# Optimization experiments

Measured on AMD Instinct MI355X. Metric: run time of the kernel, lower is better.

The kernel has to match this reference:

```python
import jax, jax.numpy as jnp
import numpy as np

N_HEAD = 16

def setup_inputs() -> dict:
    key = jax.random.key(0)
    k1, k2, k3, k4 = jax.random.split(key, 4)
    B, S, D = 2, 2048, 1024
    seq_in = jax.random.normal(k1, (B, S, D), dtype=jnp.float32)
    # nn.Linear weights, shape [out_features, in_features], y = x @ W.T
    scale = 1.0 / np.sqrt(D)
    Wq = jax.random.normal(k2, (D, D), dtype=jnp.float32) * scale
    Wk = jax.random.normal(k3, (D, D), dtype=jnp.float32) * scale
    Wv = jax.random.normal(k4, (D, D), dtype=jnp.float32) * scale
    return {"seq_in": seq_in, "Wq": Wq, "Wk": Wk, "Wv": Wv}

def reference(seq_in, Wq, Wk, Wv):
    B, S, D = seq_in.shape
    H = N_HEAD
    Dh = D // H
    scale = float(D) ** 0.5  # NOTE: sqrt(model_dim), as in the source
    # Linear projections: y = x @ W.T
    q = jnp.einsum('bsd,ed->bse', seq_in, Wq)
    k = jnp.einsum('bsd,ed->bse', seq_in, Wk)
    v = jnp.einsum('bsd,ed->bse', seq_in, Wv)
    # Faithful to source: .view(B, n_head, -1, head_dim) splits the SEQ dim,
    # not a transpose-based head split.
    q = q.reshape(B, H, S, Dh)
    k = k.reshape(B, H, S, Dh)
    v = v.reshape(B, H, S, Dh)
    sim_score = jnp.einsum('bhqd,bhkd->bhqk', q, k) / scale  # [B,H,S,S]
    sim_score = jax.nn.softmax(sim_score, axis=-1)
    # dropout is identity in eval mode
    self_attn = jnp.einsum('bhqk,bhkd->bhqd', sim_score, v)  # [B,H,S,Dh]
    self_attn = jnp.transpose(self_attn, (0, 2, 1, 3)).reshape(B, S, H * Dh)
    return (self_attn, sim_score)
```

## Files before the change

kernel.cpp:

```cpp
#include <hip/hip_runtime.h>
#include <hip/hip_bf16.h>

typedef __attribute__((ext_vector_type(8))) short short8;
typedef __attribute__((ext_vector_type(4))) float f32x4;
typedef __attribute__((ext_vector_type(4))) unsigned short u16x4;
typedef __attribute__((ext_vector_type(8))) unsigned short u16x8;

#define INV_SCALE 0.03125f

__device__ __forceinline__ unsigned short f2bf(float f) {
  unsigned u = __float_as_uint(f);
  u += 0x7fffu + ((u >> 16) & 1u);
  return (unsigned short)(u >> 16);
}

__global__ __launch_bounds__(512) void qkv_proj(
    const float* __restrict__ X, const float* __restrict__ Wq,
    const float* __restrict__ Wk, const float* __restrict__ Wv,
    unsigned short* __restrict__ ws) {
  const int mt = blockIdx.x, nt = blockIdx.y, z = blockIdx.z;
  const float* __restrict__ W = (z == 0) ? Wq : (z == 1) ? Wk : Wv;
  unsigned short* __restrict__ out = ws + (size_t)z * 4096 * 1024;

  __shared__ unsigned short As[128][72];
  __shared__ unsigned short Bs[128][72];

  const int tid = threadIdx.x;
  const int wave = tid >> 6, lane = tid & 63;
  const int lq = lane & 15, lg = lane >> 4;

  f32x4 acc[8] = {};

  for (int kt = 0; kt < 1024; kt += 64) {
    {
      const int row0 = tid >> 4;
      const int col  = (tid & 15) * 4;
#pragma unroll
      for (int i = 0; i < 4; ++i) {
        const int row = row0 + 32 * i;
        float4 a = *(const float4*)(X + (size_t)(mt * 128 + row) * 1024 + kt + col);
        float4 b = *(const float4*)(W + (size_t)(nt * 128 + row) * 1024 + kt + col);
        u16x4 ah = {f2bf(a.x), f2bf(a.y), f2bf(a.z), f2bf(a.w)};
        u16x4 bh = {f2bf(b.x), f2bf(b.y), f2bf(b.z), f2bf(b.w)};
        *(u16x4*)&As[row][col] = ah;
        *(u16x4*)&Bs[row][col] = bh;
      }
    }
    __syncthreads();
#pragma unroll
    for (int ks = 0; ks < 2; ++ks) {
      short8 af = *(const short8*)&As[wave * 16 + lq][ks * 32 + lg * 8];
#pragma unroll
      for (int n = 0; n < 8; ++n) {
        short8 bf = *(const short8*)&Bs[n * 16 + lq][ks * 32 + lg * 8];
        acc[n] = __builtin_amdgcn_mfma_f32_16x16x32_bf16(af, bf, acc[n], 0, 0, 0);
      }
    }
    __syncthreads();
  }
#pragma unroll
  for (int n = 0; n < 8; ++n)
#pragma unroll
    for (int r = 0; r < 4; ++r) {
      const int row = mt * 128 + wave * 16 + lg * 4 + r;
      const int col = nt * 128 + n * 16 + lq;
      out[(size_t)row * 1024 + col] = f2bf(acc[n][r]);
    }
}

__global__ __launch_bounds__(512) void mha_attn(
    const unsigned short* __restrict__ ws, float* __restrict__ out) {
  const int qb = blockIdx.x;
  const int bh = blockIdx.y;
  const int b = bh >> 4, h = bh & 15;

  const unsigned short* __restrict__ Qg = ws + ((size_t)b * 2048 + h * 128) * 1024;
  const unsigned short* __restrict__ Kg = Qg + (size_t)4096 * 1024;
  const unsigned short* __restrict__ Vg = Qg + (size_t)2 * 4096 * 1024;

  float* __restrict__ simout =
      out + (size_t)4194304 + ((size_t)bh * 2048 + (size_t)qb * 128) * 2048;
  float* __restrict__ attnout = out + (size_t)b * 2048 * 1024 + h * 64;

  __shared__ unsigned short Ks[128][72];
  __shared__ unsigned short VTs[64][136];
  __shared__ unsigned short Ps[8][16][136];

  const int tid = threadIdx.x;
  const int wave = tid >> 6, lane = tid & 63;
  const int lq = lane & 15, lg = lane >> 4;

  short8 qf[2];
  {
    const unsigned short* qrow = Qg + (size_t)(qb * 128 + wave * 16 + lq) * 64;
    qf[0] = *(const short8*)(qrow + lg * 8);
    qf[1] = *(const short8*)(qrow + 32 + lg * 8);
  }

  float m[4], l[4];
#pragma unroll
  for (int r = 0; r < 4; ++r) { m[r] = -1e30f; l[r] = 0.f; }

  for (int kt = 0; kt < 16; ++kt) {
#pragma unroll
    for (int i = 0; i < 2; ++i) {
      const int slot = tid + 512 * i;
      const int row = slot >> 3, cg = (slot & 7) * 8;
      u16x8 v = *(const u16x8*)(Kg + (size_t)(kt * 128 + row) * 64 + cg);
      *(u16x8*)&Ks[row][cg] = v;
    }
    __syncthreads();
    f32x4 acc[8] = {};
#pragma unroll
    for (int ks = 0; ks < 2; ++ks)
#pragma unroll
      for (int n = 0; n < 8; ++n) {
        short8 kf = *(const short8*)&Ks[n * 16 + lq][ks * 32 + lg * 8];
        acc[n] = __builtin_amdgcn_mfma_f32_16x16x32_bf16(qf[ks], kf, acc[n], 0, 0, 0);
      }
#pragma unroll
    for (int r = 0; r < 4; ++r) {
      float v = acc[0][r];
#pragma unroll
      for (int n = 1; n < 8; ++n) v = fmaxf(v, acc[n][r]);
#pragma unroll
      for (int off = 1; off < 16; off <<= 1) v = fmaxf(v, __shfl_xor(v, off));
      const float mn = fmaxf(m[r], v * INV_SCALE);
      float s = 0.f;
#pragma unroll
      for (int n = 0; n < 8; ++n) s += __expf(acc[n][r] * INV_SCALE - mn);
#pragma unroll
      for (int off = 1; off < 16; off <<= 1) s += __shfl_xor(s, off);
      l[r] = l[r] * __expf(m[r] - mn) + s;
      m[r] = mn;
    }
    __syncthreads();
  }

  float linv[4];
#pragma unroll
  for (int r = 0; r < 4; ++r) linv[r] = 1.0f / l[r];

  f32x4 oacc[4] = {};

  for (int kt = 0; kt < 16; ++kt) {
#pragma unroll
    for (int i = 0; i < 2; ++i) {
      const int slot = tid + 512 * i;
      const int row = slot >> 3, cg = (slot & 7) * 8;
      u16x8 v = *(const u16x8*)(Kg + (size_t)(kt * 128 + row) * 64 + cg);
      *(u16x8*)&Ks[row][cg] = v;
    }
    {
      const int k0 = (tid >> 3) * 2, cg = (tid & 7) * 8;
      u16x8 va = *(const u16x8*)(Vg + (size_t)(kt * 128 + k0) * 64 + cg);
      u16x8 vb = *(const u16x8*)(Vg + (size_t)(kt * 128 + k0 + 1) * 64 + cg);
#pragma unroll
      for (int j = 0; j < 8; ++j) {
        unsigned val = (unsigned)va[j] | ((unsigned)vb[j] << 16);
        *(unsigned*)&VTs[cg + j][k0] = val;
      }
    }
    __syncthreads();
    f32x4 acc[8] = {};
#pragma unroll
    for (int ks = 0; ks < 2; ++ks)
#pragma unroll
      for (int n = 0; n < 8; ++n) {
        short8 kf = *(const short8*)&Ks[n * 16 + lq][ks * 32 + lg * 8];
        acc[n] = __builtin_amdgcn_mfma_f32_16x16x32_bf16(qf[ks], kf, acc[n], 0, 0, 0);
      }
#pragma unroll
    for (int n = 0; n < 8; ++n)
#pragma unroll
      for (int r = 0; r < 4; ++r) {
        const float p = __expf(acc[n][r] * INV_SCALE - m[r]) * linv[r];
        simout[(size_t)(wave * 16 + lg * 4 + r) * 2048 + kt * 128 + n * 16 + lq] = p;
        Ps[wave][lg * 4 + r][n * 16 + lq] = f2bf(p);
      }
#pragma unroll
    for (int d = 0; d < 4; ++d)
#pragma unroll
      for (int ks = 0; ks < 4; ++ks) {
        short8 pf = *(const short8*)&Ps[wave][lq][ks * 32 + lg * 8];
        short8 vf = *(const short8*)&VTs[d * 16 + lq][ks * 32 + lg * 8];
        oacc[d] = __builtin_amdgcn_mfma_f32_16x16x32_bf16(pf, vf, oacc[d], 0, 0, 0);
      }
    __syncthreads();
  }
#pragma unroll
  for (int d = 0; d < 4; ++d)
#pragma unroll
    for (int r = 0; r < 4; ++r) {
      attnout[(size_t)(qb * 128 + wave * 16 + lg * 4 + r) * 1024 + d * 16 + lq] =
          oacc[d][r];
    }
}

extern "C" void kernel_launch(void* const* d_in, const int* in_sizes, int n_in,
                              void* d_out, int out_size, void* d_ws, size_t ws_size,
                              hipStream_t stream) {
  const float* X  = (const float*)d_in[0];
  const float* Wq = (const float*)d_in[1];
  const float* Wk = (const float*)d_in[2];
  const float* Wv = (const float*)d_in[3];
  unsigned short* ws = (unsigned short*)d_ws;
  float* out = (float*)d_out;

  qkv_proj<<<dim3(32, 8, 3), 512, 0, stream>>>(X, Wq, Wk, Wv, ws);
  mha_attn<<<dim3(16, 32), 512, 0, stream>>>(ws, out);
}
```

Measured before the change: 757.8 us.

## Retile QKV GEMM to 2x2 waves and transpose QK^T MFMA for vectorized prob stores

The projection kernel now runs 256 threads with a 2x2 wave grid, each wave computing a 64x64 sub-tile so LDS fragments are reused across four MFMAs. It also uses packed bf16 conversion and folds the 1/32 score scale into Q at write time. The attention kernel swaps the MFMA operand order so each lane holds one query row, which reduces the row max and sum to two shuffles and allows float4 stores of the fp32 probability matrix. Softmax now uses exp2 with a log2e prescale, and launch bounds request higher occupancy, which risks register spills.

```diff
diff --git a/kernel.cpp b/kernel.cpp
--- a/kernel.cpp
+++ b/kernel.cpp
@@ -3,24 +3,28 @@
 
 typedef __attribute__((ext_vector_type(8))) short short8;
 typedef __attribute__((ext_vector_type(4))) float f32x4;
-typedef __attribute__((ext_vector_type(4))) unsigned short u16x4;
 typedef __attribute__((ext_vector_type(8))) unsigned short u16x8;
 
-#define INV_SCALE 0.03125f
+#define LOG2E 1.4426950408889634f
+
+__device__ __forceinline__ unsigned pk2(float a, float b) {
+  __hip_bfloat162 h = __float22bfloat162_rn(float2{a, b});
+  return *reinterpret_cast<unsigned*>(&h);
+}
 
 __device__ __forceinline__ unsigned short f2bf(float f) {
-  unsigned u = __float_as_uint(f);
-  u += 0x7fffu + ((u >> 16) & 1u);
-  return (unsigned short)(u >> 16);
-}
-
-__global__ __launch_bounds__(512) void qkv_proj(
+  __hip_bfloat16 h = __float2bfloat16(f);
+  return *reinterpret_cast<unsigned short*>(&h);
+}
+
+__global__ __launch_bounds__(256, 3) void qkv_proj(
     const float* __restrict__ X, const float* __restrict__ Wq,
     const float* __restrict__ Wk, const float* __restrict__ Wv,
     unsigned short* __restrict__ ws) {
   const int mt = blockIdx.x, nt = blockIdx.y, z = blockIdx.z;
   const float* __restrict__ W = (z == 0) ? Wq : (z == 1) ? Wk : Wv;
   unsigned short* __restrict__ out = ws + (size_t)z * 4096 * 1024;
+  const float osc = (z == 0) ? 0.03125f : 1.0f;
 
   __shared__ unsigned short As[128][72];
   __shared__ unsigned short Bs[128][72];
@@ -28,47 +32,52 @@
   const int tid = threadIdx.x;
   const int wave = tid >> 6, lane = tid & 63;
   const int lq = lane & 15, lg = lane >> 4;
-
-  f32x4 acc[8] = {};
+  const int wr = wave >> 1, wc = wave & 1;
+
+  f32x4 acc[4][4] = {};
+
+  const int srow = tid >> 4;
+  const int sc4 = (tid & 15) * 4;
 
   for (int kt = 0; kt < 1024; kt += 64) {
-    {
-      const int row0 = tid >> 4;
-      const int col  = (tid & 15) * 4;
+#pragma unroll
+    for (int i = 0; i < 8; ++i) {
+      const int row = srow + 16 * i;
+      float4 a = *(const float4*)(X + (size_t)(mt * 128 + row) * 1024 + kt + sc4);
+      float4 b = *(const float4*)(W + (size_t)(nt * 128 + row) * 1024 + kt + sc4);
+      *(uint2*)&As[row][sc4] = make_uint2(pk2(a.x, a.y), pk2(a.z, a.w));
+      *(uint2*)&Bs[row][sc4] = make_uint2(pk2(b.x, b.y), pk2(b.z, b.w));
+    }
+    __syncthreads();
+#pragma unroll
+    for (int ks = 0; ks < 2; ++ks) {
+      short8 af[4], bf[4];
 #pragma unroll
       for (int i = 0; i < 4; ++i) {
-        const int row = row0 + 32 * i;
-        float4 a = *(const float4*)(X + (size_t)(mt * 128 + row) * 1024 + kt + col);
-        float4 b = *(const float4*)(W + (size_t)(nt * 128 + row) * 1024 + kt + col);
-        u16x4 ah = {f2bf(a.x), f2bf(a.y), f2bf(a.z), f2bf(a.w)};
-        u16x4 bh = {f2bf(b.x), f2bf(b.y), f2bf(b.z), f2bf(b.w)};
-        *(u16x4*)&As[row][col] = ah;
-        *(u16x4*)&Bs[row][col] = bh;
-      }
-    }
-    __syncthreads();
-#pragma unroll
-    for (int ks = 0; ks < 2; ++ks) {
-      short8 af = *(const short8*)&As[wave * 16 + lq][ks * 32 + lg * 8];
-#pragma unroll
-      for (int n = 0; n < 8; ++n) {
-        short8 bf = *(const short8*)&Bs[n * 16 + lq][ks * 32 + lg * 8];
-        acc[n] = __builtin_amdgcn_mfma_f32_16x16x32_bf16(af, bf, acc[n], 0, 0, 0);
-      }
-    }
-    __syncthreads();
-  }
-#pragma unroll
-  for (int n = 0; n < 8; ++n)
-#pragma unroll
-    for (int r = 0; r < 4; ++r) {
-      const int row = mt * 128 + wave * 16 + lg * 4 + r;
-      const int col = nt * 128 + n * 16 + lq;
-      out[(size_t)row * 1024 + col] = f2bf(acc[n][r]);
-    }
-}
-
-__global__ __launch_bounds__(512) void mha_attn(
+        af[i] = *(const short8*)&As[wr * 64 + i * 16 + lq][ks * 32 + lg * 8];
+        bf[i] = *(const short8*)&Bs[wc * 64 + i * 16 + lq][ks * 32 + lg * 8];
+      }
+#pragma unroll
+      for (int i = 0; i < 4; ++i)
+#pragma unroll
+        for (int j = 0; j < 4; ++j)
+          acc[i][j] = __builtin_amdgcn_mfma_f32_16x16x32_bf16(af[i], bf[j], acc[i][j], 0, 0, 0);
+    }
+    __syncthreads();
+  }
+#pragma unroll
+  for (int i = 0; i < 4; ++i)
+#pragma unroll
+    for (int j = 0; j < 4; ++j)
+#pragma unroll
+      for (int r = 0; r < 4; ++r) {
+        const int row = mt * 128 + wr * 64 + i * 16 + lg * 4 + r;
+        const int col = nt * 128 + wc * 64 + j * 16 + lq;
+        out[(size_t)row * 1024 + col] = f2bf(acc[i][j][r] * osc);
+      }
+}
+
+__global__ __launch_bounds__(512, 4) void mha_attn(
     const unsigned short* __restrict__ ws, float* __restrict__ out) {
   const int qb = blockIdx.x;
   const int bh = blockIdx.y;
@@ -97,17 +106,14 @@
     qf[1] = *(const short8*)(qrow + 32 + lg * 8);
   }
 
-  float m[4], l[4];
-#pragma unroll
-  for (int r = 0; r < 4; ++r) { m[r] = -1e30f; l[r] = 0.f; }
+  float m = -1e30f, l = 0.f;
 
   for (int kt = 0; kt < 16; ++kt) {
 #pragma unroll
     for (int i = 0; i < 2; ++i) {
       const int slot = tid + 512 * i;
       const int row = slot >> 3, cg = (slot & 7) * 8;
-      u16x8 v = *(const u16x8*)(Kg + (size_t)(kt * 128 + row) * 64 + cg);
-      *(u16x8*)&Ks[row][cg] = v;
+      *(u16x8*)&Ks[row][cg] = *(const u16x8*)(Kg + (size_t)(kt * 128 + row) * 64 + cg);
     }
     __syncthreads();
     f32x4 acc[8] = {};
@@ -116,30 +122,32 @@
 #pragma unroll
       for (int n = 0; n < 8; ++n) {
         short8 kf = *(const short8*)&Ks[n * 16 + lq][ks * 32 + lg * 8];
-        acc[n] = __builtin_amdgcn_mfma_f32_16x16x32_bf16(qf[ks], kf, acc[n], 0, 0, 0);
-      }
-#pragma unroll
-    for (int r = 0; r < 4; ++r) {
-      float v = acc[0][r];
-#pragma unroll
-      for (int n = 1; n < 8; ++n) v = fmaxf(v, acc[n][r]);
-#pragma unroll
-      for (int off = 1; off < 16; off <<= 1) v = fmaxf(v, __shfl_xor(v, off));
-      const float mn = fmaxf(m[r], v * INV_SCALE);
-      float s = 0.f;
-#pragma unroll
-      for (int n = 0; n < 8; ++n) s += __expf(acc[n][r] * INV_SCALE - mn);
-#pragma unroll
-      for (int off = 1; off < 16; off <<= 1) s += __shfl_xor(s, off);
-      l[r] = l[r] * __expf(m[r] - mn) + s;
-      m[r] = mn;
-    }
-    __syncthreads();
-  }
-
-  float linv[4];
-#pragma unroll
-  for (int r = 0; r < 4; ++r) linv[r] = 1.0f / l[r];
+        acc[n] = __builtin_amdgcn_mfma_f32_16x16x32_bf16(kf, qf[ks], acc[n], 0, 0, 0);
+      }
+    float mx = acc[0][0];
+#pragma unroll
+    for (int n = 0; n < 8; ++n)
+#pragma unroll
+      for (int r = 0; r < 4; ++r) mx = fmaxf(mx, acc[n][r]);
+    mx = fmaxf(mx, __shfl_xor(mx, 16));
+    mx = fmaxf(mx, __shfl_xor(mx, 32));
+    const float mn = fmaxf(m, mx);
+    const float m2 = mn * LOG2E;
+    float s = 0.f;
+#pragma unroll
+    for (int n = 0; n < 8; ++n)
+#pragma unroll
+      for (int r = 0; r < 4; ++r)
+        s += __builtin_amdgcn_exp2f(acc[n][r] * LOG2E - m2);
+    s += __shfl_xor(s, 16);
+    s += __shfl_xor(s, 32);
+    l = l * __builtin_amdgcn_exp2f(m * LOG2E - m2) + s;
+    m = mn;
+    __syncthreads();
+  }
+
+  const float m2f = m * LOG2E;
+  const float linv = 1.0f / l;
 
   f32x4 oacc[4] = {};
 
@@ -148,8 +156,7 @@
     for (int i = 0; i < 2; ++i) {
       const int slot = tid + 512 * i;
       const int row = slot >> 3, cg = (slot & 7) * 8;
-      u16x8 v = *(const u16x8*)(Kg + (size_t)(kt * 128 + row) * 64 + cg);
-      *(u16x8*)&Ks[row][cg] = v;
+      *(u16x8*)&Ks[row][cg] = *(const u16x8*)(Kg + (size_t)(kt * 128 + row) * 64 + cg);
     }
     {
       const int k0 = (tid >> 3) * 2, cg = (tid & 7) * 8;
@@ -157,7 +164,7 @@
       u16x8 vb = *(const u16x8*)(Vg + (size_t)(kt * 128 + k0 + 1) * 64 + cg);
 #pragma unroll
       for (int j = 0; j < 8; ++j) {
-        unsigned val = (unsigned)va[j] | ((unsigned)vb[j] << 16);
+        unsigned val = (unsigned)(unsigned short)va[j] | ((unsigned)(unsigned short)vb[j] << 16);
         *(unsigned*)&VTs[cg + j][k0] = val;
       }
     }
@@ -168,24 +175,28 @@
 #pragma unroll
       for (int n = 0; n < 8; ++n) {
         short8 kf = *(const short8*)&Ks[n * 16 + lq][ks * 32 + lg * 8];
-        acc[n] = __builtin_amdgcn_mfma_f32_16x16x32_bf16(qf[ks], kf, acc[n], 0, 0, 0);
-      }
-#pragma unroll
-    for (int n = 0; n < 8; ++n)
-#pragma unroll
-      for (int r = 0; r < 4; ++r) {
-        const float p = __expf(acc[n][r] * INV_SCALE - m[r]) * linv[r];
-        simout[(size_t)(wave * 16 + lg * 4 + r) * 2048 + kt * 128 + n * 16 + lq] = p;
-        Ps[wave][lg * 4 + r][n * 16 + lq] = f2bf(p);
-      }
-#pragma unroll
-    for (int d = 0; d < 4; ++d)
-#pragma unroll
-      for (int ks = 0; ks < 4; ++ks) {
-        short8 pf = *(const short8*)&Ps[wave][lq][ks * 32 + lg * 8];
+        acc[n] = __builtin_amdgcn_mfma_f32_16x16x32_bf16(kf, qf[ks], acc[n], 0, 0, 0);
+      }
+    float* simrow = simout + (size_t)(wave * 16 + lq) * 2048 + kt * 128 + lg * 4;
+#pragma unroll
+    for (int n = 0; n < 8; ++n) {
+      float4 p;
+      p.x = __builtin_amdgcn_exp2f(acc[n][0] * LOG2E - m2f) * linv;
+      p.y = __builtin_amdgcn_exp2f(acc[n][1] * LOG2E - m2f) * linv;
+      p.z = __builtin_amdgcn_exp2f(acc[n][2] * LOG2E - m2f) * linv;
+      p.w = __builtin_amdgcn_exp2f(acc[n][3] * LOG2E - m2f) * linv;
+      *(float4*)(simrow + n * 16) = p;
+      *(uint2*)&Ps[wave][lq][n * 16 + lg * 4] = make_uint2(pk2(p.x, p.y), pk2(p.z, p.w));
+    }
+#pragma unroll
+    for (int ks = 0; ks < 4; ++ks) {
+      short8 pf = *(const short8*)&Ps[wave][lq][ks * 32 + lg * 8];
+#pragma unroll
+      for (int d = 0; d < 4; ++d) {
         short8 vf = *(const short8*)&VTs[d * 16 + lq][ks * 32 + lg * 8];
         oacc[d] = __builtin_amdgcn_mfma_f32_16x16x32_bf16(pf, vf, oacc[d], 0, 0, 0);
       }
+    }
     __syncthreads();
   }
 #pragma unroll
@@ -207,6 +218,6 @@
   unsigned short* ws = (unsigned short*)d_ws;
   float* out = (float*)d_out;
 
-  qkv_proj<<<dim3(32, 8, 3), 512, 0, stream>>>(X, Wq, Wk, Wv, ws);
+  qkv_proj<<<dim3(32, 8, 3), 256, 0, stream>>>(X, Wq, Wk, Wv, ws);
   mha_attn<<<dim3(16, 32), 512, 0, stream>>>(ws, out);
 }
```

Measured after the change: 704.8 us. 7.0% less time.
